# Optimization experiments

Measured on AMD Instinct MI355X. Metric: run time of the kernel, lower is better.

The kernel has to match this reference:

```python
import jax, jax.numpy as jnp
import numpy as np

N_IN = 1024
N_OUT = 1024
BATCH = 8192
N_GRID = 10  # grid_points = linspace(-1, 1, 10); 9 segments
LN_EPS = 1e-5


def setup_inputs() -> dict:
    key = jax.random.key(0)
    k = jax.random.split(key, 6)
    return {
        "x": jax.random.normal(k[0], (BATCH, N_IN), dtype=jnp.float32),
        "weights": jax.random.normal(k[1], (N_OUT, N_IN), dtype=jnp.float32) * (1.0 / np.sqrt(N_IN)),
        "biases": jax.random.normal(k[2], (N_OUT,), dtype=jnp.float32),
        "slopes": jax.random.normal(k[3], (N_OUT, N_IN, N_GRID - 1), dtype=jnp.float32) * 0.05,
        "intercepts": jax.random.normal(k[4], (N_OUT, N_IN, N_GRID - 1), dtype=jnp.float32) * 0.05,
        "prelu_weight": jnp.full((1,), 0.25, dtype=jnp.float32),
    }


def reference(x, weights, biases, slopes, intercepts, prelu_weight):
    grid = jnp.linspace(-1.0, 1.0, N_GRID, dtype=x.dtype)
    n_seg = N_GRID - 1

    # base branch: GELU (exact, matching torch nn.GELU default) then linear
    b_out = jax.nn.gelu(x, approximate=False) @ weights.T + biases  # [B, n_out]

    # segment index per (sample, input feature)
    pos = (x[..., None] - grid) >= 0  # [B, n_in, N_GRID]
    seg = jnp.clip(jnp.sum(pos.astype(jnp.int32), axis=-1) - 1, 0, n_seg - 1)  # [B, n_in]

    # Faithful to torch.gather semantics: only slopes[:, 0, :] / intercepts[:, 0, :]
    # are read (index dim-2 has size 1 -> j==0). The piecewise sum over n_in then
    # reduces to segment-sums of x and segment counts contracted with those slices.
    onehot = jax.nn.one_hot(seg, n_seg, dtype=x.dtype)  # [B, n_in, n_seg]
    seg_x = jnp.einsum('bis,bi->bs', onehot, x)          # sum of x per segment
    seg_cnt = jnp.sum(onehot, axis=1)                    # count per segment
    slopes0 = slopes[:, 0, :]        # [n_out, n_seg]
    icpt0 = intercepts[:, 0, :]      # [n_out, n_seg]
    lin = seg_x @ slopes0.T + seg_cnt @ icpt0.T          # [B, n_out]

    y = b_out + lin
    # LayerNorm over n_out, no affine
    mu = jnp.mean(y, axis=-1, keepdims=True)
    var = jnp.mean(jnp.square(y - mu), axis=-1, keepdims=True)
    yn = (y - mu) * jax.lax.rsqrt(var + LN_EPS)
    # PReLU with single shared weight
    return jnp.where(yn >= 0, yn, prelu_weight * yn)
```

## Files before the change

### kernel.cpp

```cpp
#include <hip/hip_runtime.h>
#include <hip/hip_fp8.h>

#define N_IN 1024
#define N_OUT 1024
#define BATCHN 8192

typedef __attribute__((ext_vector_type(4))) int intx4;
typedef __attribute__((ext_vector_type(8))) int intx8;
typedef __attribute__((ext_vector_type(16))) float floatx16;
typedef __attribute__((ext_vector_type(2))) float f32x2;

__device__ __forceinline__ unsigned short f2bf(float f) {
  unsigned int u = __float_as_uint(f);
  u += 0x7FFFu + ((u >> 16) & 1u);
  return (unsigned short)(u >> 16);
}
__device__ __forceinline__ float bf2f(unsigned short s) {
  return __uint_as_float(((unsigned int)s) << 16);
}
__device__ __forceinline__ unsigned int f2e4m3(float f) {
  __hip_fp8_e4m3 v(f);
  return (unsigned int)v.__x;
}
__device__ __forceinline__ float gelu_fast(float v) {
  float e = __builtin_amdgcn_exp2f(-2.4554443f * v);
  return v * __builtin_amdgcn_rcpf(1.0f + e);
}

__global__ __launch_bounds__(256) void prep_all(const float* __restrict__ x,
                                                unsigned char* __restrict__ g8,
                                                float* __restrict__ seg,
                                                const float* __restrict__ W,
                                                unsigned char* __restrict__ Wb8,
                                                const float* __restrict__ slopes,
                                                const float* __restrict__ icpts,
                                                float* __restrict__ slt,
                                                float* __restrict__ ict) {
  const int b = blockIdx.x;
  const int t = threadIdx.x;
  if (b < BATCHN / 4) {
    const int lane = t & 63, wv = t >> 6;
    const int row = b * 4 + wv;
    const float* xr = x + row * N_IN;
    unsigned int* gr = (unsigned int*)(g8 + row * N_IN);
    float cum[8], cumx[8], totx = 0.f;
#pragma unroll
    for (int s = 0; s < 8; ++s) { cum[s] = 0.f; cumx[s] = 0.f; }
#pragma unroll
    for (int j = 0; j < 4; ++j) {
      float4 v4 = ((const float4*)xr)[lane + 64 * j];
      float vs[4] = {v4.x, v4.y, v4.z, v4.w};
      unsigned int pk = 0;
#pragma unroll
      for (int e = 0; e < 4; ++e) {
        float v = vs[e];
        pk |= f2e4m3(gelu_fast(v) * 4.0f) << (8 * e);
        totx += v;
#pragma unroll
        for (int k = 0; k < 8; ++k) {
          bool m = v >= (-1.0f + (float)(k + 1) * (2.0f / 9.0f));
          cum[k] += m ? 1.0f : 0.0f;
          cumx[k] += m ? v : 0.0f;
        }
      }
      gr[lane + 64 * j] = pk;
    }
#pragma unroll
    for (int off = 32; off > 0; off >>= 1) {
      totx += __shfl_xor(totx, off);
#pragma unroll
      for (int s = 0; s < 8; ++s) {
        cum[s] += __shfl_xor(cum[s], off);
        cumx[s] += __shfl_xor(cumx[s], off);
      }
    }
    if (lane == 0) {
      float sx[9], sc[9];
      sx[0] = totx - cumx[0];
      sc[0] = 1024.f - cum[0];
#pragma unroll
      for (int s = 1; s < 8; ++s) {
        sx[s] = cumx[s - 1] - cumx[s];
        sc[s] = cum[s - 1] - cum[s];
      }
      sx[8] = cumx[7];
      sc[8] = cum[7];
#pragma unroll
      for (int s = 0; s < 9; ++s) {
        seg[row * 18 + s] = sx[s];
        seg[row * 18 + 9 + s] = sc[s];
      }
    }
  } else if (b < BATCHN / 4 + N_OUT) {
    const int o = b - BATCHN / 4;
    float4 v = ((const float4*)(W + o * N_IN))[t];
    unsigned int pk = f2e4m3(v.x * 16.0f) | (f2e4m3(v.y * 16.0f) << 8) |
                      (f2e4m3(v.z * 16.0f) << 16) | (f2e4m3(v.w * 16.0f) << 24);
    ((unsigned int*)(Wb8 + o * N_IN))[t] = pk;
  } else {
    const int gb = b - (BATCHN / 4 + N_OUT);
    const int o = gb * 16 + (t >> 4);
    const int s = t & 15;
    if (s < 9) {
      slt[s * N_OUT + o] = slopes[(long)o * 9216 + s];
      ict[s * N_OUT + o] = icpts[(long)o * 9216 + s];
    }
  }
}

#define ASYNC_CP16(gp, lp)                                                     \
  __builtin_amdgcn_global_load_lds(                                            \
      (const __attribute__((address_space(1))) unsigned int*)(gp),             \
      (__attribute__((address_space(3))) unsigned int*)(lp), 16, 0, 0)

__global__ __launch_bounds__(256) void gemm_bt(const unsigned char* __restrict__ A,
                                               const unsigned char* __restrict__ B,
                                               unsigned short* __restrict__ Cb) {
  __shared__ unsigned char lA[128 * 128];
  __shared__ unsigned char lB[128 * 128];
  const int t = threadIdx.x;
  const int m0 = blockIdx.x * 128;
  const int n0 = blockIdx.y * 128;
  const int lane = t & 63, wv = t >> 6;
  const int wm = (wv >> 1) * 64, wn = (wv & 1) * 64;
  floatx16 acc[2][2] = {};

  const int l31 = lane & 31;
  const int lh = lane >> 5;

  for (int kt = 0; kt < N_IN / 128; ++kt) {
    __syncthreads();
    const int ko = kt * 128;
#pragma unroll
    for (int j = 0; j < 4; ++j) {
      const int sg = t + 256 * j;
      const int r = sg >> 3;
      const int lc = (sg & 7) ^ (r & 7);
      ASYNC_CP16(A + (m0 + r) * N_IN + ko + lc * 16, &lA[sg * 16]);
    }
#pragma unroll
    for (int j = 0; j < 4; ++j) {
      const int sg = t + 256 * j;
      const int r = sg >> 3;
      const int lc = (sg & 7) ^ (r & 7);
      ASYNC_CP16(B + (n0 + r) * N_IN + ko + lc * 16, &lB[sg * 16]);
    }
    __syncthreads();
#pragma unroll
    for (int kk = 0; kk < 2; ++kk) {
      const int lc0 = kk * 4 + lh * 2;
      intx8 af[2], bf[2];
#pragma unroll
      for (int i = 0; i < 2; ++i) {
        const int row = wm + i * 32 + l31;
        const int sw = row & 7;
        intx4 lo = *(const intx4*)&lA[row * 128 + ((lc0 ^ sw) * 16)];
        intx4 hi = *(const intx4*)&lA[row * 128 + (((lc0 + 1) ^ sw) * 16)];
        af[i][0] = lo[0]; af[i][1] = lo[1]; af[i][2] = lo[2]; af[i][3] = lo[3];
        af[i][4] = hi[0]; af[i][5] = hi[1]; af[i][6] = hi[2]; af[i][7] = hi[3];
      }
#pragma unroll
      for (int i = 0; i < 2; ++i) {
        const int row = wn + i * 32 + l31;
        const int sw = row & 7;
        intx4 lo = *(const intx4*)&lB[row * 128 + ((lc0 ^ sw) * 16)];
        intx4 hi = *(const intx4*)&lB[row * 128 + (((lc0 + 1) ^ sw) * 16)];
        bf[i][0] = lo[0]; bf[i][1] = lo[1]; bf[i][2] = lo[2]; bf[i][3] = lo[3];
        bf[i][4] = hi[0]; bf[i][5] = hi[1]; bf[i][6] = hi[2]; bf[i][7] = hi[3];
      }
#pragma unroll
      for (int mi = 0; mi < 2; ++mi)
#pragma unroll
        for (int ni = 0; ni < 2; ++ni)
          acc[mi][ni] = __builtin_amdgcn_mfma_scale_f32_32x32x64_f8f6f4(
              af[mi], bf[ni], acc[mi][ni], 0 , 0 ,
              0, 0x7D7D7D7Du , 0, 0x7B7B7B7Bu );
    }
  }

  const int lrow = 4 * lh;
#pragma unroll
  for (int mi = 0; mi < 2; ++mi)
#pragma unroll
    for (int ni = 0; ni < 2; ++ni)
#pragma unroll
      for (int rg = 0; rg < 16; ++rg) {
        const int r = m0 + wm + mi * 32 + (rg & 3) + 8 * (rg >> 2) + lrow;
        const int c = n0 + wn + ni * 32 + l31;
        Cb[r * N_OUT + c] = f2bf(acc[mi][ni][rg]);
      }
}

__global__ __launch_bounds__(512) void ln_prelu(const unsigned short* __restrict__ Cb,
                                                float* __restrict__ out,
                                                const float* __restrict__ biases,
                                                const float* __restrict__ seg,
                                                const float* __restrict__ slt,
                                                const float* __restrict__ ict,
                                                const float* __restrict__ prelu_w) {
  const int t = threadIdx.x;
  const int o = 2 * t;
  const int lane = t & 63, wv = t >> 6;
  const float2 bb = *(const float2*)&biases[o];
  float sl1[9], sl2[9], ic1[9], ic2[9];
#pragma unroll
  for (int s = 0; s < 9; ++s) {
    float2 sv = *(const float2*)&slt[s * N_OUT + o];
    float2 iv = *(const float2*)&ict[s * N_OUT + o];
    sl1[s] = sv.x; sl2[s] = sv.y;
    ic1[s] = iv.x; ic2[s] = iv.y;
  }
  const float pw = prelu_w[0];
  __shared__ float4 red[2][8];
  for (int it = 0; it < 4; ++it) {
    const int rowA = blockIdx.x * 8 + it * 2;
    const int rowB = rowA + 1;
    const float* segA = seg + rowA * 18;
    const float* segB = seg + rowB * 18;
    ushort2 ca = *(const ushort2*)&Cb[rowA * N_OUT + o];
    ushort2 cb = *(const ushort2*)&Cb[rowB * N_OUT + o];
    float ya1 = bf2f(ca.x) + bb.x, ya2 = bf2f(ca.y) + bb.y;
    float yb1 = bf2f(cb.x) + bb.x, yb2 = bf2f(cb.y) + bb.y;
#pragma unroll
    for (int s = 0; s < 9; ++s) {
      float sxa = segA[s], cta = segA[9 + s];
      float sxb = segB[s], ctb = segB[9 + s];
      ya1 += sxa * sl1[s] + cta * ic1[s];
      ya2 += sxa * sl2[s] + cta * ic2[s];
      yb1 += sxb * sl1[s] + ctb * ic1[s];
      yb2 += sxb * sl2[s] + ctb * ic2[s];
    }
    float sa = ya1 + ya2, qa = ya1 * ya1 + ya2 * ya2;
    float sb = yb1 + yb2, qb = yb1 * yb1 + yb2 * yb2;
#pragma unroll
    for (int off = 32; off > 0; off >>= 1) {
      sa += __shfl_xor(sa, off);
      qa += __shfl_xor(qa, off);
      sb += __shfl_xor(sb, off);
      qb += __shfl_xor(qb, off);
    }
    if (lane == 0) red[it & 1][wv] = make_float4(sa, qa, sb, qb);
    __syncthreads();
    float s8a = 0.f, q8a = 0.f, s8b = 0.f, q8b = 0.f;
#pragma unroll
    for (int i = 0; i < 8; ++i) {
      float4 p = red[it & 1][i];
      s8a += p.x; q8a += p.y; s8b += p.z; q8b += p.w;
    }
    const float muA = s8a * (1.0f / 1024.0f);
    const float rstdA = rsqrtf(q8a * (1.0f / 1024.0f) - muA * muA + 1e-5f);
    const float muB = s8b * (1.0f / 1024.0f);
    const float rstdB = rsqrtf(q8b * (1.0f / 1024.0f) - muB * muB + 1e-5f);
    float za1 = (ya1 - muA) * rstdA, za2 = (ya2 - muA) * rstdA;
    float zb1 = (yb1 - muB) * rstdB, zb2 = (yb2 - muB) * rstdB;
    za1 = za1 >= 0.f ? za1 : pw * za1;
    za2 = za2 >= 0.f ? za2 : pw * za2;
    zb1 = zb1 >= 0.f ? zb1 : pw * zb1;
    zb2 = zb2 >= 0.f ? zb2 : pw * zb2;
    f32x2 va = {za1, za2}, vb = {zb1, zb2};
    __builtin_nontemporal_store(va, (f32x2*)&out[rowA * N_OUT + o]);
    __builtin_nontemporal_store(vb, (f32x2*)&out[rowB * N_OUT + o]);
  }
}

extern "C" void kernel_launch(void* const* d_in, const int* in_sizes, int n_in,
                              void* d_out, int out_size, void* d_ws, size_t ws_size,
                              hipStream_t stream) {
  const float* x = (const float*)d_in[0];
  const float* W = (const float*)d_in[1];
  const float* biases = (const float*)d_in[2];
  const float* slopes = (const float*)d_in[3];
  const float* icpts = (const float*)d_in[4];
  const float* prelu_w = (const float*)d_in[5];
  float* out = (float*)d_out;

  char* ws = (char*)d_ws;
  unsigned char* g8 = (unsigned char*)ws;
  unsigned char* Wb8 = (unsigned char*)(ws + (8u << 20));
  unsigned short* Cb = (unsigned short*)(ws + (16u << 20));
  float* seg = (float*)(ws + (33u << 20));
  float* slt = (float*)(ws + (34u << 20));
  float* ict = (float*)(ws + (34u << 20) + (64u << 10));

  prep_all<<<BATCHN / 4 + N_OUT + 64, 256, 0, stream>>>(x, g8, seg, W, Wb8, slopes,
                                                        icpts, slt, ict);
  gemm_bt<<<dim3(BATCHN / 128, N_OUT / 128), 256, 0, stream>>>(g8, Wb8, Cb);
  ln_prelu<<<BATCHN / 8, 512, 0, stream>>>(Cb, out, biases, seg, slt, ict, prelu_w);
}
```

Before: 166.0 us.

## Fuse activation prep, FP8 GEMM and LayerNorm-PReLU into one row-block kernel

Replaces the three-kernel pipeline (x prep, tiled GEMM, LN/PReLU) with a weight-prep kernel plus one fused kernel. Each 512-thread block handles 32 full rows: it quantizes GELU(x) to FP8 straight into LDS, computes the segment sums there, and runs the full N_OUT=1024 MFMA GEMM with each wave covering 128 columns. It then adds the bias and piecewise terms and applies LayerNorm and PReLU in registers before writing the output. This removes the global round trips for the FP8 activations, the bf16 intermediate C and the seg buffer, but B is now read directly from global/L2 without LDS staging, and the grid has only 256 blocks with large LDS use.

```diff
diff --git a/kernel.cpp b/kernel.cpp
--- a/kernel.cpp
+++ b/kernel.cpp
@@ -8,16 +8,7 @@
 typedef __attribute__((ext_vector_type(4))) int intx4;
 typedef __attribute__((ext_vector_type(8))) int intx8;
 typedef __attribute__((ext_vector_type(16))) float floatx16;
-typedef __attribute__((ext_vector_type(2))) float f32x2;
-
-__device__ __forceinline__ unsigned short f2bf(float f) {
-  unsigned int u = __float_as_uint(f);
-  u += 0x7FFFu + ((u >> 16) & 1u);
-  return (unsigned short)(u >> 16);
-}
-__device__ __forceinline__ float bf2f(unsigned short s) {
-  return __uint_as_float(((unsigned int)s) << 16);
-}
+
 __device__ __forceinline__ unsigned int f2e4m3(float f) {
   __hip_fp8_e4m3 v(f);
   return (unsigned int)v.__x;
@@ -27,28 +18,57 @@
   return v * __builtin_amdgcn_rcpf(1.0f + e);
 }
 
-__global__ __launch_bounds__(256) void prep_all(const float* __restrict__ x,
-                                                unsigned char* __restrict__ g8,
-                                                float* __restrict__ seg,
-                                                const float* __restrict__ W,
-                                                unsigned char* __restrict__ Wb8,
-                                                const float* __restrict__ slopes,
-                                                const float* __restrict__ icpts,
-                                                float* __restrict__ slt,
-                                                float* __restrict__ ict) {
-  const int b = blockIdx.x;
+__global__ __launch_bounds__(256) void prep_w(const float* __restrict__ W,
+                                              unsigned char* __restrict__ Wb8,
+                                              const float* __restrict__ slopes,
+                                              const float* __restrict__ icpts,
+                                              float* __restrict__ slt,
+                                              float* __restrict__ ict) {
+  const int b = blockIdx.x, t = threadIdx.x;
+  if (b < N_OUT) {
+    float4 v = ((const float4*)(W + b * N_IN))[t];
+    unsigned int pk = f2e4m3(v.x * 16.0f) | (f2e4m3(v.y * 16.0f) << 8) |
+                      (f2e4m3(v.z * 16.0f) << 16) | (f2e4m3(v.w * 16.0f) << 24);
+    ((unsigned int*)(Wb8 + b * N_IN))[t] = pk;
+  } else {
+    const int gb = b - N_OUT;
+    const int o = gb * 16 + (t >> 4);
+    const int s = t & 15;
+    if (s < 9) {
+      slt[s * N_OUT + o] = slopes[(long)o * 9216 + s];
+      ict[s * N_OUT + o] = icpts[(long)o * 9216 + s];
+    }
+  }
+}
+
+__global__ __launch_bounds__(512) void fused(const float* __restrict__ x,
+                                             const unsigned char* __restrict__ Wb8,
+                                             const float* __restrict__ biases,
+                                             const float* __restrict__ slt,
+                                             const float* __restrict__ ict,
+                                             const float* __restrict__ prelu_w,
+                                             float* __restrict__ out) {
+  __shared__ unsigned char lA[32 * 1024];
+  __shared__ float seg_lds[32][24];
+  __shared__ float2 red[8][32];
+  __shared__ float2 rowstat[32];
+
   const int t = threadIdx.x;
-  if (b < BATCHN / 4) {
-    const int lane = t & 63, wv = t >> 6;
-    const int row = b * 4 + wv;
-    const float* xr = x + row * N_IN;
-    unsigned int* gr = (unsigned int*)(g8 + row * N_IN);
+  const int lane = t & 63, w = t >> 6;
+  const int l31 = lane & 31, lh = lane >> 5;
+  const int r0 = blockIdx.x * 32;
+
+  for (int jr = 0; jr < 4; ++jr) {
+    const int rl = 4 * w + jr;
+    const float* xr = x + (r0 + rl) * N_IN;
+    unsigned int* lrow = (unsigned int*)(lA + rl * 1024);
+    const int sw = rl & 7;
     float cum[8], cumx[8], totx = 0.f;
 #pragma unroll
     for (int s = 0; s < 8; ++s) { cum[s] = 0.f; cumx[s] = 0.f; }
 #pragma unroll
-    for (int j = 0; j < 4; ++j) {
-      float4 v4 = ((const float4*)xr)[lane + 64 * j];
+    for (int jc = 0; jc < 4; ++jc) {
+      float4 v4 = ((const float4*)xr)[lane + 64 * jc];
       float vs[4] = {v4.x, v4.y, v4.z, v4.w};
       unsigned int pk = 0;
 #pragma unroll
@@ -63,7 +83,8 @@
           cumx[k] += m ? v : 0.0f;
         }
       }
-      gr[lane + 64 * j] = pk;
+      const int d = lane + 64 * jc;
+      lrow[(((d >> 2) ^ sw) << 2) | (d & 3)] = pk;
     }
 #pragma unroll
     for (int off = 32; off > 0; off >>= 1) {
@@ -75,191 +96,125 @@
       }
     }
     if (lane == 0) {
-      float sx[9], sc[9];
-      sx[0] = totx - cumx[0];
-      sc[0] = 1024.f - cum[0];
+      seg_lds[rl][0] = totx - cumx[0];
+      seg_lds[rl][12] = 1024.f - cum[0];
 #pragma unroll
       for (int s = 1; s < 8; ++s) {
-        sx[s] = cumx[s - 1] - cumx[s];
-        sc[s] = cum[s - 1] - cum[s];
+        seg_lds[rl][s] = cumx[s - 1] - cumx[s];
+        seg_lds[rl][12 + s] = cum[s - 1] - cum[s];
       }
-      sx[8] = cumx[7];
-      sc[8] = cum[7];
-#pragma unroll
-      for (int s = 0; s < 9; ++s) {
-        seg[row * 18 + s] = sx[s];
-        seg[row * 18 + 9 + s] = sc[s];
-      }
-    }
-  } else if (b < BATCHN / 4 + N_OUT) {
-    const int o = b - BATCHN / 4;
-    float4 v = ((const float4*)(W + o * N_IN))[t];
-    unsigned int pk = f2e4m3(v.x * 16.0f) | (f2e4m3(v.y * 16.0f) << 8) |
-                      (f2e4m3(v.z * 16.0f) << 16) | (f2e4m3(v.w * 16.0f) << 24);
-    ((unsigned int*)(Wb8 + o * N_IN))[t] = pk;
-  } else {
-    const int gb = b - (BATCHN / 4 + N_OUT);
-    const int o = gb * 16 + (t >> 4);
-    const int s = t & 15;
-    if (s < 9) {
-      slt[s * N_OUT + o] = slopes[(long)o * 9216 + s];
-      ict[s * N_OUT + o] = icpts[(long)o * 9216 + s];
-    }
-  }
-}
-
-#define ASYNC_CP16(gp, lp)                                                     \
-  __builtin_amdgcn_global_load_lds(                                            \
-      (const __attribute__((address_space(1))) unsigned int*)(gp),             \
-      (__attribute__((address_space(3))) unsigned int*)(lp), 16, 0, 0)
-
-__global__ __launch_bounds__(256) void gemm_bt(const unsigned char* __restrict__ A,
-                                               const unsigned char* __restrict__ B,
-                                               unsigned short* __restrict__ Cb) {
-  __shared__ unsigned char lA[128 * 128];
-  __shared__ unsigned char lB[128 * 128];
-  const int t = threadIdx.x;
-  const int m0 = blockIdx.x * 128;
-  const int n0 = blockIdx.y * 128;
-  const int lane = t & 63, wv = t >> 6;
-  const int wm = (wv >> 1) * 64, wn = (wv & 1) * 64;
-  floatx16 acc[2][2] = {};
-
-  const int l31 = lane & 31;
-  const int lh = lane >> 5;
-
-  for (int kt = 0; kt < N_IN / 128; ++kt) {
-    __syncthreads();
-    const int ko = kt * 128;
-#pragma unroll
-    for (int j = 0; j < 4; ++j) {
-      const int sg = t + 256 * j;
-      const int r = sg >> 3;
-      const int lc = (sg & 7) ^ (r & 7);
-      ASYNC_CP16(A + (m0 + r) * N_IN + ko + lc * 16, &lA[sg * 16]);
-    }
-#pragma unroll
-    for (int j = 0; j < 4; ++j) {
-      const int sg = t + 256 * j;
-      const int r = sg >> 3;
-      const int lc = (sg & 7) ^ (r & 7);
-      ASYNC_CP16(B + (n0 + r) * N_IN + ko + lc * 16, &lB[sg * 16]);
-    }
-    __syncthreads();
-#pragma unroll
-    for (int kk = 0; kk < 2; ++kk) {
-      const int lc0 = kk * 4 + lh * 2;
-      intx8 af[2], bf[2];
-#pragma unroll
-      for (int i = 0; i < 2; ++i) {
-        const int row = wm + i * 32 + l31;
-        const int sw = row & 7;
-        intx4 lo = *(const intx4*)&lA[row * 128 + ((lc0 ^ sw) * 16)];
-        intx4 hi = *(const intx4*)&lA[row * 128 + (((lc0 + 1) ^ sw) * 16)];
-        af[i][0] = lo[0]; af[i][1] = lo[1]; af[i][2] = lo[2]; af[i][3] = lo[3];
-        af[i][4] = hi[0]; af[i][5] = hi[1]; af[i][6] = hi[2]; af[i][7] = hi[3];
-      }
-#pragma unroll
-      for (int i = 0; i < 2; ++i) {
-        const int row = wn + i * 32 + l31;
-        const int sw = row & 7;
-        intx4 lo = *(const intx4*)&lB[row * 128 + ((lc0 ^ sw) * 16)];
-        intx4 hi = *(const intx4*)&lB[row * 128 + (((lc0 + 1) ^ sw) * 16)];
-        bf[i][0] = lo[0]; bf[i][1] = lo[1]; bf[i][2] = lo[2]; bf[i][3] = lo[3];
-        bf[i][4] = hi[0]; bf[i][5] = hi[1]; bf[i][6] = hi[2]; bf[i][7] = hi[3];
-      }
-#pragma unroll
-      for (int mi = 0; mi < 2; ++mi)
-#pragma unroll
-        for (int ni = 0; ni < 2; ++ni)
-          acc[mi][ni] = __builtin_amdgcn_mfma_scale_f32_32x32x64_f8f6f4(
-              af[mi], bf[ni], acc[mi][ni], 0 , 0 ,
-              0, 0x7D7D7D7Du , 0, 0x7B7B7B7Bu );
-    }
-  }
-
-  const int lrow = 4 * lh;
-#pragma unroll
-  for (int mi = 0; mi < 2; ++mi)
-#pragma unroll
-    for (int ni = 0; ni < 2; ++ni)
-#pragma unroll
-      for (int rg = 0; rg < 16; ++rg) {
-        const int r = m0 + wm + mi * 32 + (rg & 3) + 8 * (rg >> 2) + lrow;
-        const int c = n0 + wn + ni * 32 + l31;
-        Cb[r * N_OUT + c] = f2bf(acc[mi][ni][rg]);
-      }
-}
-
-__global__ __launch_bounds__(512) void ln_prelu(const unsigned short* __restrict__ Cb,
-                                                float* __restrict__ out,
-                                                const float* __restrict__ biases,
-                                                const float* __restrict__ seg,
-                                                const float* __restrict__ slt,
-                                                const float* __restrict__ ict,
-                                                const float* __restrict__ prelu_w) {
-  const int t = threadIdx.x;
-  const int o = 2 * t;
-  const int lane = t & 63, wv = t >> 6;
-  const float2 bb = *(const float2*)&biases[o];
-  float sl1[9], sl2[9], ic1[9], ic2[9];
-#pragma unroll
-  for (int s = 0; s < 9; ++s) {
-    float2 sv = *(const float2*)&slt[s * N_OUT + o];
-    float2 iv = *(const float2*)&ict[s * N_OUT + o];
-    sl1[s] = sv.x; sl2[s] = sv.y;
-    ic1[s] = iv.x; ic2[s] = iv.y;
+      seg_lds[rl][8] = cumx[7];
+      seg_lds[rl][20] = cum[7];
+    }
+  }
+  __syncthreads();
+
+  const int nb = w * 128;
+  floatx16 acc[4] = {};
+  const unsigned char* aRow = lA + l31 * 1024;
+  const int asw = l31 & 7;
+  const unsigned char* bp0 = Wb8 + (nb + l31) * N_IN + lh * 32;
+
+#define LOAD_A(ko, AF)                                                         \
+  {                                                                            \
+    const int c0 = ((ko) >> 4) + lh * 2;                                       \
+    intx4 lo = *(const intx4*)(aRow + ((c0 ^ asw) << 4));                      \
+    intx4 hi = *(const intx4*)(aRow + (((c0 + 1) ^ asw) << 4));                \
+    AF[0] = lo[0]; AF[1] = lo[1]; AF[2] = lo[2]; AF[3] = lo[3];                \
+    AF[4] = hi[0]; AF[5] = hi[1]; AF[6] = hi[2]; AF[7] = hi[3];                \
+  }
+#define LOAD_B(ko, ni, BF)                                                     \
+  {                                                                            \
+    const unsigned char* bp = bp0 + (ni) * 32 * N_IN + (ko);                   \
+    intx4 lo = *(const intx4*)bp;                                              \
+    intx4 hi = *(const intx4*)(bp + 16);                                       \
+    BF[0] = lo[0]; BF[1] = lo[1]; BF[2] = lo[2]; BF[3] = lo[3];                \
+    BF[4] = hi[0]; BF[5] = hi[1]; BF[6] = hi[2]; BF[7] = hi[3];                \
+  }
+
+  for (int kt = 0; kt < 16; kt += 2) {
+    intx8 a0, a1, b0[4], b1[4];
+    LOAD_A(kt * 64, a0);
+    LOAD_A(kt * 64 + 64, a1);
+#pragma unroll
+    for (int ni = 0; ni < 4; ++ni) LOAD_B(kt * 64, ni, b0[ni]);
+#pragma unroll
+    for (int ni = 0; ni < 4; ++ni) LOAD_B(kt * 64 + 64, ni, b1[ni]);
+#pragma unroll
+    for (int ni = 0; ni < 4; ++ni)
+      acc[ni] = __builtin_amdgcn_mfma_scale_f32_32x32x64_f8f6f4(
+          a0, b0[ni], acc[ni], 0, 0, 0, 0x7D7D7D7Du , 0,
+          0x7B7B7B7Bu );
+#pragma unroll
+    for (int ni = 0; ni < 4; ++ni)
+      acc[ni] = __builtin_amdgcn_mfma_scale_f32_32x32x64_f8f6f4(
+          a1, b1[ni], acc[ni], 0, 0, 0, 0x7D7D7D7Du, 0, 0x7B7B7B7Bu);
+  }
+
+  float bb[4], cs[4][9], ci[4][9];
+#pragma unroll
+  for (int ni = 0; ni < 4; ++ni) {
+    const int c = nb + ni * 32 + l31;
+    bb[ni] = biases[c];
+#pragma unroll
+    for (int s = 0; s < 9; ++s) {
+      cs[ni][s] = slt[s * N_OUT + c];
+      ci[ni][s] = ict[s * N_OUT + c];
+    }
+  }
+
+#pragma unroll
+  for (int rg = 0; rg < 16; ++rg) {
+    const int rl = (rg & 3) + 8 * (rg >> 2) + 4 * lh;
+    float sx[9], sc[9];
+#pragma unroll
+    for (int s = 0; s < 9; ++s) {
+      sx[s] = seg_lds[rl][s];
+      sc[s] = seg_lds[rl][12 + s];
+    }
+    float ssum = 0.f, qsum = 0.f;
+#pragma unroll
+    for (int ni = 0; ni < 4; ++ni) {
+      float y = acc[ni][rg] + bb[ni];
+#pragma unroll
+      for (int s = 0; s < 9; ++s) y += sx[s] * cs[ni][s] + sc[s] * ci[ni][s];
+      acc[ni][rg] = y;
+      ssum += y;
+      qsum += y * y;
+    }
+#pragma unroll
+    for (int off = 16; off > 0; off >>= 1) {
+      ssum += __shfl_xor(ssum, off);
+      qsum += __shfl_xor(qsum, off);
+    }
+    if (l31 == 0) red[w][rl] = make_float2(ssum, qsum);
+  }
+  __syncthreads();
+  if (t < 32) {
+    float s = 0.f, q = 0.f;
+#pragma unroll
+    for (int wv = 0; wv < 8; ++wv) {
+      float2 p = red[wv][t];
+      s += p.x;
+      q += p.y;
+    }
+    const float mu = s * (1.0f / 1024.0f);
+    const float rstd = rsqrtf(q * (1.0f / 1024.0f) - mu * mu + 1e-5f);
+    rowstat[t] = make_float2(mu, rstd);
   }
   const float pw = prelu_w[0];
-  __shared__ float4 red[2][8];
-  for (int it = 0; it < 4; ++it) {
-    const int rowA = blockIdx.x * 8 + it * 2;
-    const int rowB = rowA + 1;
-    const float* segA = seg + rowA * 18;
-    const float* segB = seg + rowB * 18;
-    ushort2 ca = *(const ushort2*)&Cb[rowA * N_OUT + o];
-    ushort2 cb = *(const ushort2*)&Cb[rowB * N_OUT + o];
-    float ya1 = bf2f(ca.x) + bb.x, ya2 = bf2f(ca.y) + bb.y;
-    float yb1 = bf2f(cb.x) + bb.x, yb2 = bf2f(cb.y) + bb.y;
-#pragma unroll
-    for (int s = 0; s < 9; ++s) {
-      float sxa = segA[s], cta = segA[9 + s];
-      float sxb = segB[s], ctb = segB[9 + s];
-      ya1 += sxa * sl1[s] + cta * ic1[s];
-      ya2 += sxa * sl2[s] + cta * ic2[s];
-      yb1 += sxb * sl1[s] + ctb * ic1[s];
-      yb2 += sxb * sl2[s] + ctb * ic2[s];
-    }
-    float sa = ya1 + ya2, qa = ya1 * ya1 + ya2 * ya2;
-    float sb = yb1 + yb2, qb = yb1 * yb1 + yb2 * yb2;
-#pragma unroll
-    for (int off = 32; off > 0; off >>= 1) {
-      sa += __shfl_xor(sa, off);
-      qa += __shfl_xor(qa, off);
-      sb += __shfl_xor(sb, off);
-      qb += __shfl_xor(qb, off);
-    }
-    if (lane == 0) red[it & 1][wv] = make_float4(sa, qa, sb, qb);
-    __syncthreads();
-    float s8a = 0.f, q8a = 0.f, s8b = 0.f, q8b = 0.f;
-#pragma unroll
-    for (int i = 0; i < 8; ++i) {
-      float4 p = red[it & 1][i];
-      s8a += p.x; q8a += p.y; s8b += p.z; q8b += p.w;
-    }
-    const float muA = s8a * (1.0f / 1024.0f);
-    const float rstdA = rsqrtf(q8a * (1.0f / 1024.0f) - muA * muA + 1e-5f);
-    const float muB = s8b * (1.0f / 1024.0f);
-    const float rstdB = rsqrtf(q8b * (1.0f / 1024.0f) - muB * muB + 1e-5f);
-    float za1 = (ya1 - muA) * rstdA, za2 = (ya2 - muA) * rstdA;
-    float zb1 = (yb1 - muB) * rstdB, zb2 = (yb2 - muB) * rstdB;
-    za1 = za1 >= 0.f ? za1 : pw * za1;
-    za2 = za2 >= 0.f ? za2 : pw * za2;
-    zb1 = zb1 >= 0.f ? zb1 : pw * zb1;
-    zb2 = zb2 >= 0.f ? zb2 : pw * zb2;
-    f32x2 va = {za1, za2}, vb = {zb1, zb2};
-    __builtin_nontemporal_store(va, (f32x2*)&out[rowA * N_OUT + o]);
-    __builtin_nontemporal_store(vb, (f32x2*)&out[rowB * N_OUT + o]);
+  __syncthreads();
+#pragma unroll
+  for (int rg = 0; rg < 16; ++rg) {
+    const int rl = (rg & 3) + 8 * (rg >> 2) + 4 * lh;
+    const float2 ms = rowstat[rl];
+    float* orow = out + (r0 + rl) * N_OUT;
+#pragma unroll
+    for (int ni = 0; ni < 4; ++ni) {
+      float z = (acc[ni][rg] - ms.x) * ms.y;
+      z = z >= 0.f ? z : pw * z;
+      __builtin_nontemporal_store(z, &orow[nb + ni * 32 + l31]);
+    }
   }
 }
 
@@ -275,15 +230,10 @@
   float* out = (float*)d_out;
 
   char* ws = (char*)d_ws;
-  unsigned char* g8 = (unsigned char*)ws;
-  unsigned char* Wb8 = (unsigned char*)(ws + (8u << 20));
-  unsigned short* Cb = (unsigned short*)(ws + (16u << 20));
-  float* seg = (float*)(ws + (33u << 20));
-  float* slt = (float*)(ws + (34u << 20));
-  float* ict = (float*)(ws + (34u << 20) + (64u << 10));
-
-  prep_all<<<BATCHN / 4 + N_OUT + 64, 256, 0, stream>>>(x, g8, seg, W, Wb8, slopes,
-                                                        icpts, slt, ict);
-  gemm_bt<<<dim3(BATCHN / 128, N_OUT / 128), 256, 0, stream>>>(g8, Wb8, Cb);
-  ln_prelu<<<BATCHN / 8, 512, 0, stream>>>(Cb, out, biases, seg, slt, ict, prelu_w);
-}
+  unsigned char* Wb8 = (unsigned char*)ws;
+  float* slt = (float*)(ws + (2u << 20));
+  float* ict = (float*)(ws + (2u << 20) + (64u << 10));
+
+  prep_w<<<N_OUT + 64, 256, 0, stream>>>(W, Wb8, slopes, icpts, slt, ict);
+  fused<<<BATCHN / 32, 512, 0, stream>>>(x, Wb8, biases, slt, ict, prelu_w, out);
+}
```

Measured after the change: 184.1 us. 1.11x slower.
